# Kernel tuning notes

Hardware: AMD Instinct MI355X
Metric: run time of the kernel (lower is better)

Reference implementation:

```python
import jax, jax.numpy as jnp
import numpy as np

N_TOKENS = 8192
D_MODEL = 1024
D_HIDDEN = 2 * D_MODEL
N_EXPERTS = 16
TOP_K = 2


def setup_inputs() -> dict:
    key = jax.random.key(0)
    ks = jax.random.split(key, 6)
    s_in = 1.0 / np.sqrt(D_MODEL)
    s_hid = 1.0 / np.sqrt(D_HIDDEN)
    return {
        "x": jax.random.normal(ks[0], (N_TOKENS, D_MODEL), dtype=jnp.float32),
        # gate: Linear(d_model, n_experts, bias=False); stored as [E, d] like torch weight
        "Wg": jax.random.uniform(ks[1], (N_EXPERTS, D_MODEL), jnp.float32, -s_in, s_in),
        # per-expert MLP params, stacked on leading expert axis; W laid out [in, out]
        "W1": jax.random.uniform(ks[2], (N_EXPERTS, D_MODEL, D_HIDDEN), jnp.float32, -s_in, s_in),
        "b1": jax.random.uniform(ks[3], (N_EXPERTS, D_HIDDEN), jnp.float32, -s_in, s_in),
        "W2": jax.random.uniform(ks[4], (N_EXPERTS, D_HIDDEN, D_MODEL), jnp.float32, -s_hid, s_hid),
        "b2": jax.random.uniform(ks[5], (N_EXPERTS, D_MODEL), jnp.float32, -s_hid, s_hid),
    }


def reference(x, Wg, W1, b1, W2, b2):
    # Router: top-k logits, softmax over the k selected logits (in fp32)
    logits = x @ Wg.T                                  # [N, E]
    topk_vals, topk_idx = jax.lax.top_k(logits, TOP_K)  # [N, K]
    rw = jax.nn.softmax(topk_vals.astype(jnp.float32), axis=-1).astype(x.dtype)
    # Combine top-k weights into per-(token, expert) weights [N, E]
    cw = (jax.nn.one_hot(topk_idx, N_EXPERTS, dtype=x.dtype) * rw[..., None]).sum(axis=1)
    # Dense per-expert MLP, weighted combine (equivalent to gather/scatter index_add_)
    out = jnp.zeros_like(x)
    for e in range(N_EXPERTS):
        h = jax.nn.relu(x @ W1[e] + b1[e])             # [N, D_HIDDEN]
        out = out + (h @ W2[e] + b2[e]) * cw[:, e:e + 1]
    return out
```

## Files before the change

### kernel.cpp

```cpp
#include <hip/hip_runtime.h>
#include <hip/hip_bf16.h>
#include <stdint.h>

#define NTOK 8192
#define DM   1024
#define DH   2048
#define NE   16

#define NWRK  768
#define QCAP1 2048
#define QCAP2 1024

typedef float  f32x4  __attribute__((ext_vector_type(4)));
typedef __bf16 bf16x8 __attribute__((ext_vector_type(8)));

__device__ __forceinline__ unsigned short f2bf(float f) {
  union { __bf16 b; unsigned short u; } c; c.b = (__bf16)f; return c.u;
}

__device__ __forceinline__ void glds16(const void* g, void* l) {
  __builtin_amdgcn_global_load_lds(
      (const __attribute__((address_space(1))) void*)g,
      (__attribute__((address_space(3))) void*)l, 16, 0, 0);
}

__global__ __launch_bounds__(256) void router_kernel(
    const float* __restrict__ x, const float* __restrict__ Wg,
    unsigned short* __restrict__ xb, int* __restrict__ eidx,
    float* __restrict__ ewt)
{
  const int lane = threadIdx.x & 63;
  const int wave = threadIdx.x >> 6;
  const int t = blockIdx.x * 4 + wave;
  const float* xr = x + (size_t)t * DM;

  float4 xv[4];
#pragma unroll
  for (int c = 0; c < 4; ++c)
    xv[c] = *(const float4*)(xr + c * 256 + lane * 4);

  unsigned short* xbr = xb + (size_t)t * DM;
#pragma unroll
  for (int c = 0; c < 4; ++c) {
    ushort4 u;
    u.x = f2bf(xv[c].x); u.y = f2bf(xv[c].y);
    u.z = f2bf(xv[c].z); u.w = f2bf(xv[c].w);
    *(ushort4*)(xbr + c * 256 + lane * 4) = u;
  }

  float acc[NE];
#pragma unroll
  for (int e = 0; e < NE; ++e) acc[e] = 0.f;
#pragma unroll
  for (int e = 0; e < NE; ++e) {
#pragma unroll
    for (int c = 0; c < 4; ++c) {
      float4 wv = *(const float4*)(Wg + e * DM + c * 256 + lane * 4);
      acc[e] += xv[c].x * wv.x + xv[c].y * wv.y + xv[c].z * wv.z + xv[c].w * wv.w;
    }
  }
#pragma unroll
  for (int e = 0; e < NE; ++e) {
    float v = acc[e];
    v += __shfl_xor(v, 1);  v += __shfl_xor(v, 2);  v += __shfl_xor(v, 4);
    v += __shfl_xor(v, 8);  v += __shfl_xor(v, 16); v += __shfl_xor(v, 32);
    acc[e] = v;
  }
  if (lane == 0) {
    float v0 = -1e30f; int i0 = 0;
#pragma unroll
    for (int e = 0; e < NE; ++e) if (acc[e] > v0) { v0 = acc[e]; i0 = e; }
    float v1 = -1e30f; int i1 = 0;
#pragma unroll
    for (int e = 0; e < NE; ++e) if (e != i0 && acc[e] > v1) { v1 = acc[e]; i1 = e; }
    float p = expf(v1 - v0);
    float s = 1.f / (1.f + p);
    eidx[2 * t] = i0; eidx[2 * t + 1] = i1;
    ewt[2 * t] = s;   ewt[2 * t + 1] = p * s;
  }
}

__global__ __launch_bounds__(1024) void plan_kernel(
    const int* __restrict__ eidx, const float* __restrict__ ewt,
    int* __restrict__ cnt, int* __restrict__ offv,
    int* __restrict__ tok, float* __restrict__ wtl,
    int* __restrict__ wl1, int* __restrict__ wl2,
    int* __restrict__ qn1, int* __restrict__ qn2,
    int* __restrict__ qc1, int* __restrict__ qc2)
{
  __shared__ int wcnt[16][NE];
  __shared__ int wbase[16][NE];
  __shared__ int offs[NE];
  __shared__ int s_nmt[NE];
  __shared__ int s_pnmt[NE + 1];

  const int tid  = threadIdx.x;
  const int wave = tid >> 6;
  const int lane = tid & 63;
  const unsigned long long below = (1ull << lane) - 1ull;

  int   pe[16];
  float pw[16];
  int   count[NE];
#pragma unroll
  for (int e = 0; e < NE; ++e) count[e] = 0;
#pragma unroll
  for (int r = 0; r < 16; ++r) {
    int p = wave * 1024 + r * 64 + lane;
    pe[r] = eidx[p];
    pw[r] = ewt[p];
#pragma unroll
    for (int e = 0; e < NE; ++e) {
      unsigned long long m = __ballot(pe[r] == e);
      count[e] += (int)__popcll(m);
    }
  }
  if (lane == 0) {
#pragma unroll
    for (int e = 0; e < NE; ++e) wcnt[wave][e] = count[e];
  }
  __syncthreads();

  if (tid == 0) {
    int s = 0;
    s_pnmt[0] = 0;
    for (int e = 0; e < NE; ++e) {
      offs[e] = s;
      int t = 0;
      for (int w = 0; w < 16; ++w) { wbase[w][e] = t; t += wcnt[w][e]; }
      cnt[e] = t; offv[e] = s; s += t;
      int nmt = (t + 127) >> 7;
      s_nmt[e] = nmt;
      s_pnmt[e + 1] = s_pnmt[e] + nmt;
    }
    offv[NE] = s;
  }
  __syncthreads();

  if (tid < 8) {
    qn1[tid] = (s_nmt[tid] + s_nmt[tid + 8]) * 16;
    qn2[tid] = (s_nmt[tid] + s_nmt[tid + 8]) * 8;
    qc1[tid] = 0;
    qc2[tid] = 0;
  }

  {
    const int totmt = s_pnmt[NE];
    const int T1 = totmt * 16;
    for (int i = tid; i < T1; i += 1024) {
      int gmt = i >> 4, p = i & 15;
      int e = 0;
      while (s_pnmt[e + 1] <= gmt) ++e;
      int mt  = gmt - s_pnmt[e];
      int nmt = s_nmt[e];
      int x    = e & 7;
      int base = (e < 8) ? 0 : s_nmt[e - 8] * 16;
      wl1[x * QCAP1 + base + p * nmt + mt] = (e << 16) | (mt << 8) | p;
    }
    const int T2 = totmt * 8;
    for (int i = tid; i < T2; i += 1024) {
      int gmt = i >> 3, p = i & 7;
      int e = 0;
      while (s_pnmt[e + 1] <= gmt) ++e;
      int mt  = gmt - s_pnmt[e];
      int nmt = s_nmt[e];
      int h0  = (nmt + 1) >> 1;
      int pos_e = (mt < h0) ? (p * h0 + mt)
                            : (h0 * 8 + p * (nmt - h0) + (mt - h0));
      int x    = e & 7;
      int base = (e < 8) ? 0 : s_nmt[e - 8] * 8;
      wl2[x * QCAP2 + base + pos_e] = (e << 16) | (mt << 8) | p;
    }
  }

  int run[NE];
#pragma unroll
  for (int e = 0; e < NE; ++e) run[e] = 0;
#pragma unroll
  for (int r = 0; r < 16; ++r) {
    int p = wave * 1024 + r * 64 + lane;
#pragma unroll
    for (int e = 0; e < NE; ++e) {
      unsigned long long m = __ballot(pe[r] == e);
      if (pe[r] == e) {
        int rank = (int)__popcll(m & below);
        int slot = offs[e] + wbase[wave][e] + run[e] + rank;
        tok[slot] = p >> 1;
        wtl[slot] = pw[r];
      }
      run[e] += (int)__popcll(m);
    }
  }
}

__global__ __launch_bounds__(256) void wprep_kernel(
    const float* __restrict__ W, unsigned short* __restrict__ WT,
    int K, int N)
{
  __shared__ float t[64][68];
  const int e = blockIdx.z;
  const int k0 = blockIdx.y * 64;
  const int n0 = blockIdx.x * 64;
  const int tid = threadIdx.x;
  const int tr = tid >> 2;
  const int tc = (tid & 3) * 16;
  const float* src = W + ((size_t)e * K + k0) * N + n0;
#pragma unroll
  for (int j = 0; j < 4; ++j) {
    float4 v = *(const float4*)(src + (size_t)tr * N + tc + j * 4);
    t[tc + j * 4 + 0][tr] = v.x;
    t[tc + j * 4 + 1][tr] = v.y;
    t[tc + j * 4 + 2][tr] = v.z;
    t[tc + j * 4 + 3][tr] = v.w;
  }
  __syncthreads();
  unsigned short* dst = WT + ((size_t)e * N + n0) * K + k0;
#pragma unroll
  for (int j = 0; j < 4; ++j) {
    float4 v = *(const float4*)(&t[tr][tc + j * 4]);
    ushort4 u;
    u.x = f2bf(v.x); u.y = f2bf(v.y); u.z = f2bf(v.z); u.w = f2bf(v.w);
    *(ushort4*)(dst + (size_t)tr * K + tc + j * 4) = u;
  }
}

template<int GATHER, int EPI, int KDIM, int NDIM, int QCAP>
__global__ __launch_bounds__(256, 3) void gemm_kernel(
    const unsigned short* __restrict__ Abase,
    const unsigned short* __restrict__ BT,
    const float* __restrict__ bias,
    const int* __restrict__ cnt, const int* __restrict__ offv,
    const int* __restrict__ tok, const float* __restrict__ wtl,
    const int* __restrict__ wl, const int* __restrict__ qn,
    int* __restrict__ qc, void* __restrict__ outp)
{
  __shared__ unsigned short Al[128 * 64];
  __shared__ unsigned short Bl[128 * 64];
  __shared__ int s_j;

  const int xcd = blockIdx.x & 7;
  const int* q_ = wl + xcd * QCAP;
  const int myqn = qn[xcd];

  const int tid  = threadIdx.x;
  const int lane = tid & 63;
  const int wave = tid >> 6;
  const int wr = wave >> 1;
  const int wc = wave & 1;

  const int lr = lane >> 3;
  const int lc = lane & 7;
  const int sc = (lc ^ lr) * 8;
  const int qq   = lane >> 4;
  const int ln15 = lane & 15;
  const int swz  = ln15 & 7;

  for (;;) {
    if (tid == 0) s_j = atomicAdd(&qc[xcd], 1);
    __syncthreads();
    const int j = s_j;
    if (j >= myqn) return;
    const int v = q_[j];

    const int e  = (v >> 16) & 0xff;
    const int m0 = ((v >> 8) & 0xff) * 128;
    const int n0 = (v & 0xff) * 128;
    const int count = cnt[e];
    const int o     = offv[e];

    const unsigned short* aptr[4];
    const unsigned short* bptr[4];
#pragma unroll
    for (int ii = 0; ii < 4; ++ii) {
      int i = wave * 4 + ii;
      int r = i * 8 + lr;
      int m = m0 + r; if (m > count - 1) m = count - 1;
      size_t arow = GATHER ? (size_t)tok[o + m] : (size_t)(o + m);
      aptr[ii] = Abase + arow * KDIM + sc;
      bptr[ii] = BT + ((size_t)e * NDIM + n0 + r) * KDIM + sc;
    }

    f32x4 acc[4][4];
#pragma unroll
    for (int a = 0; a < 4; ++a)
#pragma unroll
      for (int b = 0; b < 4; ++b) acc[a][b] = 0.f;

    for (int k0 = 0; k0 < KDIM; k0 += 64) {
#pragma unroll
      for (int ii = 0; ii < 4; ++ii) {
        int i = wave * 4 + ii;
        glds16(aptr[ii] + k0, &Al[i * 512]);
        glds16(bptr[ii] + k0, &Bl[i * 512]);
      }
      __syncthreads();
#pragma unroll
      for (int kk = 0; kk < 2; ++kk) {
        bf16x8 af[4], bg[4];
        const int ch = (kk * 4 + qq) ^ swz;
#pragma unroll
        for (int a = 0; a < 4; ++a) {
          int r = wr * 64 + a * 16 + ln15;
          af[a] = *(const bf16x8*)(&Al[r * 64 + ch * 8]);
        }
#pragma unroll
        for (int b = 0; b < 4; ++b) {
          int r = wc * 64 + b * 16 + ln15;
          bg[b] = *(const bf16x8*)(&Bl[r * 64 + ch * 8]);
        }
#pragma unroll
        for (int a = 0; a < 4; ++a)
#pragma unroll
          for (int b = 0; b < 4; ++b)
            acc[a][b] = __builtin_amdgcn_mfma_f32_16x16x32_bf16(af[a], bg[b], acc[a][b], 0, 0, 0);
      }
      __syncthreads();
    }

    float bn[4];
#pragma unroll
    for (int b = 0; b < 4; ++b)
      bn[b] = bias[(size_t)e * NDIM + n0 + wc * 64 + b * 16 + ln15];

    if (EPI == 0) {
      unsigned short* hout = (unsigned short*)outp;
#pragma unroll
      for (int a = 0; a < 4; ++a)
#pragma unroll
        for (int rg = 0; rg < 4; ++rg) {
          int r = wr * 64 + a * 16 + qq * 4 + rg;
          int m = m0 + r;
          if (m < count) {
            size_t slot = (size_t)(o + m);
#pragma unroll
            for (int b = 0; b < 4; ++b) {
              float v2 = acc[a][b][rg] + bn[b];
              v2 = v2 > 0.f ? v2 : 0.f;
              hout[slot * NDIM + n0 + wc * 64 + b * 16 + ln15] = f2bf(v2);
            }
          }
        }
    } else {
      float* obase = (float*)outp;
#pragma unroll
      for (int a = 0; a < 4; ++a)
#pragma unroll
        for (int rg = 0; rg < 4; ++rg) {
          int r = wr * 64 + a * 16 + qq * 4 + rg;
          int m = m0 + r;
          if (m < count) {
            int slot = o + m;
            int tk = tok[slot];
            float w = wtl[slot];
#pragma unroll
            for (int b = 0; b < 4; ++b) {
              float v2 = (acc[a][b][rg] + bn[b]) * w;
              atomicAdd(&obase[(size_t)tk * NDIM + n0 + wc * 64 + b * 16 + ln15], v2);
            }
          }
        }
    }
  }
}

extern "C" void kernel_launch(void* const* d_in, const int* in_sizes, int n_in,
                              void* d_out, int out_size, void* d_ws, size_t ws_size,
                              hipStream_t stream) {
  const float* x  = (const float*)d_in[0];
  const float* Wg = (const float*)d_in[1];
  const float* W1 = (const float*)d_in[2];
  const float* b1 = (const float*)d_in[3];
  const float* W2 = (const float*)d_in[4];
  const float* b2 = (const float*)d_in[5];

  constexpr size_t OFF_CNT  = 0;
  constexpr size_t OFF_OFF  = 256;
  constexpr size_t OFF_QN1  = 512;
  constexpr size_t OFF_QN2  = 544;
  constexpr size_t OFF_QC1  = 576;
  constexpr size_t OFF_QC2  = 608;
  constexpr size_t OFF_WL1  = 4096;
  constexpr size_t OFF_WL2  = OFF_WL1 + (size_t)8 * QCAP1 * 4;
  constexpr size_t OFF_EIDX = 131072;
  constexpr size_t OFF_EWT  = OFF_EIDX + (size_t)NTOK * 2 * 4;
  constexpr size_t OFF_TOK  = OFF_EWT  + (size_t)NTOK * 2 * 4;
  constexpr size_t OFF_WTL  = OFF_TOK  + (size_t)NTOK * 2 * 4;
  constexpr size_t OFF_XB   = (size_t)1 << 20;
  constexpr size_t OFF_W1T  = OFF_XB  + (size_t)NTOK * DM * 2;
  constexpr size_t OFF_W2T  = OFF_W1T + (size_t)NE * DM * DH * 2;
  constexpr size_t OFF_H    = OFF_W2T + (size_t)NE * DH * DM * 2;
  constexpr size_t REQ      = OFF_H   + (size_t)NTOK * 2 * DH * 2;

  if (ws_size < REQ) {
    hipMemsetAsync(d_out, 0, (size_t)out_size * 4, stream);
    return;
  }

  char* ws = (char*)d_ws;
  int*   cnt    = (int*)(ws + OFF_CNT);
  int*   offv   = (int*)(ws + OFF_OFF);
  int*   qn1    = (int*)(ws + OFF_QN1);
  int*   qn2    = (int*)(ws + OFF_QN2);
  int*   qc1    = (int*)(ws + OFF_QC1);
  int*   qc2    = (int*)(ws + OFF_QC2);
  int*   wl1    = (int*)(ws + OFF_WL1);
  int*   wl2    = (int*)(ws + OFF_WL2);
  int*   eidx   = (int*)(ws + OFF_EIDX);
  float* ewt    = (float*)(ws + OFF_EWT);
  int*   tok    = (int*)(ws + OFF_TOK);
  float* wtl    = (float*)(ws + OFF_WTL);
  unsigned short* xb   = (unsigned short*)(ws + OFF_XB);
  unsigned short* w1t  = (unsigned short*)(ws + OFF_W1T);
  unsigned short* w2t  = (unsigned short*)(ws + OFF_W2T);
  unsigned short* hbuf = (unsigned short*)(ws + OFF_H);

  hipMemsetAsync(d_out, 0, (size_t)out_size * 4, stream);

  router_kernel<<<NTOK / 4, 256, 0, stream>>>(x, Wg, xb, eidx, ewt);
  wprep_kernel<<<dim3(DH / 64, DM / 64, NE), 256, 0, stream>>>(W1, w1t, DM, DH);
  wprep_kernel<<<dim3(DM / 64, DH / 64, NE), 256, 0, stream>>>(W2, w2t, DH, DM);
  plan_kernel<<<1, 1024, 0, stream>>>(eidx, ewt, cnt, offv, tok, wtl,
                                      wl1, wl2, qn1, qn2, qc1, qc2);

  gemm_kernel<1, 0, DM, DH, QCAP1><<<NWRK, 256, 0, stream>>>(
      xb, w1t, b1, cnt, offv, tok, wtl, wl1, qn1, qc1, hbuf);
  gemm_kernel<0, 1, DH, DM, QCAP2><<<NWRK, 256, 0, stream>>>(
      hbuf, w2t, b2, cnt, offv, tok, wtl, wl2, qn2, qc2, (float*)d_out);
}
```

Before: 406.6 us.

## Use single-wave 64x64 GEMM tiles with register double-buffering, merge prep kernels

```diff
diff --git a/kernel.cpp b/kernel.cpp
--- a/kernel.cpp
+++ b/kernel.cpp
@@ -7,9 +7,9 @@
 #define DH   2048
 #define NE   16
 
-#define NWRK  768
-#define QCAP1 2048
-#define QCAP2 1024
+#define NWRK  3072
+#define QCAP1 8704
+#define QCAP2 4352
 
 typedef float  f32x4  __attribute__((ext_vector_type(4)));
 typedef __bf16 bf16x8 __attribute__((ext_vector_type(8)));
@@ -18,65 +18,101 @@
   union { __bf16 b; unsigned short u; } c; c.b = (__bf16)f; return c.u;
 }
 
-__device__ __forceinline__ void glds16(const void* g, void* l) {
-  __builtin_amdgcn_global_load_lds(
-      (const __attribute__((address_space(1))) void*)g,
-      (__attribute__((address_space(3))) void*)l, 16, 0, 0);
-}
-
-__global__ __launch_bounds__(256) void router_kernel(
+__global__ __launch_bounds__(256) void prep_kernel(
     const float* __restrict__ x, const float* __restrict__ Wg,
     unsigned short* __restrict__ xb, int* __restrict__ eidx,
-    float* __restrict__ ewt)
+    float* __restrict__ ewt,
+    const float* __restrict__ W1, unsigned short* __restrict__ w1t,
+    const float* __restrict__ W2, unsigned short* __restrict__ w2t)
 {
-  const int lane = threadIdx.x & 63;
-  const int wave = threadIdx.x >> 6;
-  const int t = blockIdx.x * 4 + wave;
-  const float* xr = x + (size_t)t * DM;
-
-  float4 xv[4];
-#pragma unroll
-  for (int c = 0; c < 4; ++c)
-    xv[c] = *(const float4*)(xr + c * 256 + lane * 4);
-
-  unsigned short* xbr = xb + (size_t)t * DM;
-#pragma unroll
-  for (int c = 0; c < 4; ++c) {
+  __shared__ float t[64][68];
+  const int bid = blockIdx.x;
+
+  if (bid < 2048) {
+    const int lane = threadIdx.x & 63;
+    const int wave = threadIdx.x >> 6;
+    const int tk = bid * 4 + wave;
+    const float* xr = x + (size_t)tk * DM;
+
+    float4 xv[4];
+#pragma unroll
+    for (int c = 0; c < 4; ++c)
+      xv[c] = *(const float4*)(xr + c * 256 + lane * 4);
+
+    unsigned short* xbr = xb + (size_t)tk * DM;
+#pragma unroll
+    for (int c = 0; c < 4; ++c) {
+      ushort4 u;
+      u.x = f2bf(xv[c].x); u.y = f2bf(xv[c].y);
+      u.z = f2bf(xv[c].z); u.w = f2bf(xv[c].w);
+      *(ushort4*)(xbr + c * 256 + lane * 4) = u;
+    }
+
+    float acc[NE];
+#pragma unroll
+    for (int e = 0; e < NE; ++e) acc[e] = 0.f;
+#pragma unroll
+    for (int e = 0; e < NE; ++e) {
+#pragma unroll
+      for (int c = 0; c < 4; ++c) {
+        float4 wv = *(const float4*)(Wg + e * DM + c * 256 + lane * 4);
+        acc[e] += xv[c].x * wv.x + xv[c].y * wv.y + xv[c].z * wv.z + xv[c].w * wv.w;
+      }
+    }
+#pragma unroll
+    for (int e = 0; e < NE; ++e) {
+      float v = acc[e];
+      v += __shfl_xor(v, 1);  v += __shfl_xor(v, 2);  v += __shfl_xor(v, 4);
+      v += __shfl_xor(v, 8);  v += __shfl_xor(v, 16); v += __shfl_xor(v, 32);
+      acc[e] = v;
+    }
+    if (lane == 0) {
+      float v0 = -1e30f; int i0 = 0;
+#pragma unroll
+      for (int e = 0; e < NE; ++e) if (acc[e] > v0) { v0 = acc[e]; i0 = e; }
+      float v1 = -1e30f; int i1 = 0;
+#pragma unroll
+      for (int e = 0; e < NE; ++e) if (e != i0 && acc[e] > v1) { v1 = acc[e]; i1 = e; }
+      float p = expf(v1 - v0);
+      float s = 1.f / (1.f + p);
+      eidx[2 * tk] = i0; eidx[2 * tk + 1] = i1;
+      ewt[2 * tk] = s;   ewt[2 * tk + 1] = p * s;
+    }
+    return;
+  }
+
+  const float* W; unsigned short* WT; int K, N, bx, by, bz;
+  if (bid < 2048 + 8192) {
+    int i = bid - 2048;
+    W = W1; WT = w1t; K = DM; N = DH;
+    bx = i & 31; by = (i >> 5) & 15; bz = i >> 9;
+  } else {
+    int i = bid - 10240;
+    W = W2; WT = w2t; K = DH; N = DM;
+    bx = i & 15; by = (i >> 4) & 31; bz = i >> 9;
+  }
+  const int k0 = by * 64;
+  const int n0 = bx * 64;
+  const int tid = threadIdx.x;
+  const int tr = tid >> 2;
+  const int tc = (tid & 3) * 16;
+  const float* src = W + ((size_t)bz * K + k0) * N + n0;
+#pragma unroll
+  for (int j = 0; j < 4; ++j) {
+    float4 v = *(const float4*)(src + (size_t)tr * N + tc + j * 4);
+    t[tc + j * 4 + 0][tr] = v.x;
+    t[tc + j * 4 + 1][tr] = v.y;
+    t[tc + j * 4 + 2][tr] = v.z;
+    t[tc + j * 4 + 3][tr] = v.w;
+  }
+  __syncthreads();
+  unsigned short* dst = WT + ((size_t)bz * N + n0) * K + k0;
+#pragma unroll
+  for (int j = 0; j < 4; ++j) {
+    float4 v = *(const float4*)(&t[tr][tc + j * 4]);
     ushort4 u;
-    u.x = f2bf(xv[c].x); u.y = f2bf(xv[c].y);
-    u.z = f2bf(xv[c].z); u.w = f2bf(xv[c].w);
-    *(ushort4*)(xbr + c * 256 + lane * 4) = u;
-  }
-
-  float acc[NE];
-#pragma unroll
-  for (int e = 0; e < NE; ++e) acc[e] = 0.f;
-#pragma unroll
-  for (int e = 0; e < NE; ++e) {
-#pragma unroll
-    for (int c = 0; c < 4; ++c) {
-      float4 wv = *(const float4*)(Wg + e * DM + c * 256 + lane * 4);
-      acc[e] += xv[c].x * wv.x + xv[c].y * wv.y + xv[c].z * wv.z + xv[c].w * wv.w;
-    }
-  }
-#pragma unroll
-  for (int e = 0; e < NE; ++e) {
-    float v = acc[e];
-    v += __shfl_xor(v, 1);  v += __shfl_xor(v, 2);  v += __shfl_xor(v, 4);
-    v += __shfl_xor(v, 8);  v += __shfl_xor(v, 16); v += __shfl_xor(v, 32);
-    acc[e] = v;
-  }
-  if (lane == 0) {
-    float v0 = -1e30f; int i0 = 0;
-#pragma unroll
-    for (int e = 0; e < NE; ++e) if (acc[e] > v0) { v0 = acc[e]; i0 = e; }
-    float v1 = -1e30f; int i1 = 0;
-#pragma unroll
-    for (int e = 0; e < NE; ++e) if (e != i0 && acc[e] > v1) { v1 = acc[e]; i1 = e; }
-    float p = expf(v1 - v0);
-    float s = 1.f / (1.f + p);
-    eidx[2 * t] = i0; eidx[2 * t + 1] = i1;
-    ewt[2 * t] = s;   ewt[2 * t + 1] = p * s;
+    u.x = f2bf(v.x); u.y = f2bf(v.y); u.z = f2bf(v.z); u.w = f2bf(v.w);
+    *(ushort4*)(dst + (size_t)tr * K + tc + j * 4) = u;
   }
 }
 
@@ -129,7 +165,7 @@
       int t = 0;
       for (int w = 0; w < 16; ++w) { wbase[w][e] = t; t += wcnt[w][e]; }
       cnt[e] = t; offv[e] = s; s += t;
-      int nmt = (t + 127) >> 7;
+      int nmt = (t + 63) >> 6;
       s_nmt[e] = nmt;
       s_pnmt[e + 1] = s_pnmt[e] + nmt;
     }
@@ -138,38 +174,38 @@
   __syncthreads();
 
   if (tid < 8) {
-    qn1[tid] = (s_nmt[tid] + s_nmt[tid + 8]) * 16;
-    qn2[tid] = (s_nmt[tid] + s_nmt[tid + 8]) * 8;
+    qn1[tid] = (s_nmt[tid] + s_nmt[tid + 8]) * 32;
+    qn2[tid] = (s_nmt[tid] + s_nmt[tid + 8]) * 16;
     qc1[tid] = 0;
     qc2[tid] = 0;
   }
 
   {
     const int totmt = s_pnmt[NE];
-    const int T1 = totmt * 16;
+    const int T1 = totmt * 32;
     for (int i = tid; i < T1; i += 1024) {
-      int gmt = i >> 4, p = i & 15;
+      int gmt = i >> 5, p = i & 31;
       int e = 0;
       while (s_pnmt[e + 1] <= gmt) ++e;
       int mt  = gmt - s_pnmt[e];
       int nmt = s_nmt[e];
-      int x    = e & 7;
-      int base = (e < 8) ? 0 : s_nmt[e - 8] * 16;
-      wl1[x * QCAP1 + base + p * nmt + mt] = (e << 16) | (mt << 8) | p;
-    }
-    const int T2 = totmt * 8;
+      int xx   = e & 7;
+      int base = (e < 8) ? 0 : s_nmt[e - 8] * 32;
+      wl1[xx * QCAP1 + base + p * nmt + mt] = (e << 24) | (mt << 12) | p;
+    }
+    const int T2 = totmt * 16;
     for (int i = tid; i < T2; i += 1024) {
-      int gmt = i >> 3, p = i & 7;
+      int gmt = i >> 4, p = i & 15;
       int e = 0;
       while (s_pnmt[e + 1] <= gmt) ++e;
       int mt  = gmt - s_pnmt[e];
       int nmt = s_nmt[e];
       int h0  = (nmt + 1) >> 1;
       int pos_e = (mt < h0) ? (p * h0 + mt)
-                            : (h0 * 8 + p * (nmt - h0) + (mt - h0));
-      int x    = e & 7;
-      int base = (e < 8) ? 0 : s_nmt[e - 8] * 8;
-      wl2[x * QCAP2 + base + pos_e] = (e << 16) | (mt << 8) | p;
+                            : (h0 * 16 + p * (nmt - h0) + (mt - h0));
+      int xx   = e & 7;
+      int base = (e < 8) ? 0 : s_nmt[e - 8] * 16;
+      wl2[xx * QCAP2 + base + pos_e] = (e << 24) | (mt << 12) | p;
     }
   }
 
@@ -193,39 +229,8 @@
   }
 }
 
-__global__ __launch_bounds__(256) void wprep_kernel(
-    const float* __restrict__ W, unsigned short* __restrict__ WT,
-    int K, int N)
-{
-  __shared__ float t[64][68];
-  const int e = blockIdx.z;
-  const int k0 = blockIdx.y * 64;
-  const int n0 = blockIdx.x * 64;
-  const int tid = threadIdx.x;
-  const int tr = tid >> 2;
-  const int tc = (tid & 3) * 16;
-  const float* src = W + ((size_t)e * K + k0) * N + n0;
-#pragma unroll
-  for (int j = 0; j < 4; ++j) {
-    float4 v = *(const float4*)(src + (size_t)tr * N + tc + j * 4);
-    t[tc + j * 4 + 0][tr] = v.x;
-    t[tc + j * 4 + 1][tr] = v.y;
-    t[tc + j * 4 + 2][tr] = v.z;
-    t[tc + j * 4 + 3][tr] = v.w;
-  }
-  __syncthreads();
-  unsigned short* dst = WT + ((size_t)e * N + n0) * K + k0;
-#pragma unroll
-  for (int j = 0; j < 4; ++j) {
-    float4 v = *(const float4*)(&t[tr][tc + j * 4]);
-    ushort4 u;
-    u.x = f2bf(v.x); u.y = f2bf(v.y); u.z = f2bf(v.z); u.w = f2bf(v.w);
-    *(ushort4*)(dst + (size_t)tr * K + tc + j * 4) = u;
-  }
-}
-
 template<int GATHER, int EPI, int KDIM, int NDIM, int QCAP>
-__global__ __launch_bounds__(256, 3) void gemm_kernel(
+__global__ __launch_bounds__(64, 3) void gemm_kernel(
     const unsigned short* __restrict__ Abase,
     const unsigned short* __restrict__ BT,
     const float* __restrict__ bias,
@@ -234,50 +239,35 @@
     const int* __restrict__ wl, const int* __restrict__ qn,
     int* __restrict__ qc, void* __restrict__ outp)
 {
-  __shared__ unsigned short Al[128 * 64];
-  __shared__ unsigned short Bl[128 * 64];
-  __shared__ int s_j;
-
-  const int xcd = blockIdx.x & 7;
-  const int* q_ = wl + xcd * QCAP;
+  const int xcd  = blockIdx.x & 7;
+  const int lane = threadIdx.x;
+  const int q    = lane >> 4;
+  const int ln15 = lane & 15;
   const int myqn = qn[xcd];
-
-  const int tid  = threadIdx.x;
-  const int lane = tid & 63;
-  const int wave = tid >> 6;
-  const int wr = wave >> 1;
-  const int wc = wave & 1;
-
-  const int lr = lane >> 3;
-  const int lc = lane & 7;
-  const int sc = (lc ^ lr) * 8;
-  const int qq   = lane >> 4;
-  const int ln15 = lane & 15;
-  const int swz  = ln15 & 7;
+  const int* q_  = wl + xcd * QCAP;
+  constexpr int KH = KDIM / 32;
 
   for (;;) {
-    if (tid == 0) s_j = atomicAdd(&qc[xcd], 1);
-    __syncthreads();
-    const int j = s_j;
+    int j = 0;
+    if (lane == 0) j = atomicAdd(&qc[xcd], 1);
+    j = __shfl(j, 0);
     if (j >= myqn) return;
     const int v = q_[j];
 
-    const int e  = (v >> 16) & 0xff;
-    const int m0 = ((v >> 8) & 0xff) * 128;
-    const int n0 = (v & 0xff) * 128;
+    const int e  = v >> 24;
+    const int m0 = ((v >> 12) & 0xfff) * 64;
+    const int n0 = (v & 0xfff) * 64;
     const int count = cnt[e];
     const int o     = offv[e];
 
-    const unsigned short* aptr[4];
-    const unsigned short* bptr[4];
-#pragma unroll
-    for (int ii = 0; ii < 4; ++ii) {
-      int i = wave * 4 + ii;
-      int r = i * 8 + lr;
-      int m = m0 + r; if (m > count - 1) m = count - 1;
+    const unsigned short* ap[4];
+    const unsigned short* bp[4];
+#pragma unroll
+    for (int a = 0; a < 4; ++a) {
+      int m = m0 + a * 16 + ln15; if (m > count - 1) m = count - 1;
       size_t arow = GATHER ? (size_t)tok[o + m] : (size_t)(o + m);
-      aptr[ii] = Abase + arow * KDIM + sc;
-      bptr[ii] = BT + ((size_t)e * NDIM + n0 + r) * KDIM + sc;
+      ap[a] = Abase + arow * KDIM + q * 8;
+      bp[a] = BT + ((size_t)e * NDIM + n0 + a * 16 + ln15) * KDIM + q * 8;
     }
 
     f32x4 acc[4][4];
@@ -286,41 +276,40 @@
 #pragma unroll
       for (int b = 0; b < 4; ++b) acc[a][b] = 0.f;
 
-    for (int k0 = 0; k0 < KDIM; k0 += 64) {
-#pragma unroll
-      for (int ii = 0; ii < 4; ++ii) {
-        int i = wave * 4 + ii;
-        glds16(aptr[ii] + k0, &Al[i * 512]);
-        glds16(bptr[ii] + k0, &Bl[i * 512]);
-      }
-      __syncthreads();
-#pragma unroll
-      for (int kk = 0; kk < 2; ++kk) {
-        bf16x8 af[4], bg[4];
-        const int ch = (kk * 4 + qq) ^ swz;
-#pragma unroll
-        for (int a = 0; a < 4; ++a) {
-          int r = wr * 64 + a * 16 + ln15;
-          af[a] = *(const bf16x8*)(&Al[r * 64 + ch * 8]);
-        }
-#pragma unroll
-        for (int b = 0; b < 4; ++b) {
-          int r = wc * 64 + b * 16 + ln15;
-          bg[b] = *(const bf16x8*)(&Bl[r * 64 + ch * 8]);
-        }
-#pragma unroll
-        for (int a = 0; a < 4; ++a)
-#pragma unroll
-          for (int b = 0; b < 4; ++b)
-            acc[a][b] = __builtin_amdgcn_mfma_f32_16x16x32_bf16(af[a], bg[b], acc[a][b], 0, 0, 0);
-      }
-      __syncthreads();
-    }
+    bf16x8 a0[4], b0[4], a1[4], b1[4];
+
+#define LOADH(A_, B_, H_) {                                               \
+    _Pragma("unroll")                                                     \
+    for (int a = 0; a < 4; ++a) {                                         \
+      A_[a] = *(const bf16x8*)(ap[a] + (H_) * 32);                        \
+      B_[a] = *(const bf16x8*)(bp[a] + (H_) * 32);                        \
+    } }
+#define MFMAH(A_, B_) {                                                   \
+    _Pragma("unroll")                                                     \
+    for (int a = 0; a < 4; ++a)                                           \
+      _Pragma("unroll")                                                   \
+      for (int b = 0; b < 4; ++b)                                         \
+        acc[a][b] = __builtin_amdgcn_mfma_f32_16x16x32_bf16(              \
+            A_[a], B_[b], acc[a][b], 0, 0, 0);                            \
+    }
+
+    LOADH(a0, b0, 0)
+    for (int kh = 0; kh < KH - 2; kh += 2) {
+      LOADH(a1, b1, kh + 1)
+      MFMAH(a0, b0)
+      LOADH(a0, b0, kh + 2)
+      MFMAH(a1, b1)
+    }
+    LOADH(a1, b1, KH - 1)
+    MFMAH(a0, b0)
+    MFMAH(a1, b1)
+#undef LOADH
+#undef MFMAH
 
     float bn[4];
 #pragma unroll
     for (int b = 0; b < 4; ++b)
-      bn[b] = bias[(size_t)e * NDIM + n0 + wc * 64 + b * 16 + ln15];
+      bn[b] = bias[(size_t)e * NDIM + n0 + b * 16 + ln15];
 
     if (EPI == 0) {
       unsigned short* hout = (unsigned short*)outp;
@@ -328,15 +317,14 @@
       for (int a = 0; a < 4; ++a)
 #pragma unroll
         for (int rg = 0; rg < 4; ++rg) {
-          int r = wr * 64 + a * 16 + qq * 4 + rg;
-          int m = m0 + r;
+          int m = m0 + a * 16 + q * 4 + rg;
           if (m < count) {
             size_t slot = (size_t)(o + m);
 #pragma unroll
             for (int b = 0; b < 4; ++b) {
               float v2 = acc[a][b][rg] + bn[b];
               v2 = v2 > 0.f ? v2 : 0.f;
-              hout[slot * NDIM + n0 + wc * 64 + b * 16 + ln15] = f2bf(v2);
+              hout[slot * NDIM + n0 + b * 16 + ln15] = f2bf(v2);
             }
           }
         }
@@ -346,8 +334,7 @@
       for (int a = 0; a < 4; ++a)
 #pragma unroll
         for (int rg = 0; rg < 4; ++rg) {
-          int r = wr * 64 + a * 16 + qq * 4 + rg;
-          int m = m0 + r;
+          int m = m0 + a * 16 + q * 4 + rg;
           if (m < count) {
             int slot = o + m;
             int tk = tok[slot];
@@ -355,7 +342,7 @@
 #pragma unroll
             for (int b = 0; b < 4; ++b) {
               float v2 = (acc[a][b][rg] + bn[b]) * w;
-              atomicAdd(&obase[(size_t)tk * NDIM + n0 + wc * 64 + b * 16 + ln15], v2);
+              atomicAdd(&obase[(size_t)tk * NDIM + n0 + b * 16 + ln15], v2);
             }
           }
         }
@@ -379,9 +366,9 @@
   constexpr size_t OFF_QN2  = 544;
   constexpr size_t OFF_QC1  = 576;
   constexpr size_t OFF_QC2  = 608;
-  constexpr size_t OFF_WL1  = 4096;
+  constexpr size_t OFF_WL1  = 8192;
   constexpr size_t OFF_WL2  = OFF_WL1 + (size_t)8 * QCAP1 * 4;
-  constexpr size_t OFF_EIDX = 131072;
+  constexpr size_t OFF_EIDX = OFF_WL2 + (size_t)8 * QCAP2 * 4;
   constexpr size_t OFF_EWT  = OFF_EIDX + (size_t)NTOK * 2 * 4;
   constexpr size_t OFF_TOK  = OFF_EWT  + (size_t)NTOK * 2 * 4;
   constexpr size_t OFF_WTL  = OFF_TOK  + (size_t)NTOK * 2 * 4;
@@ -390,6 +377,7 @@
   constexpr size_t OFF_W2T  = OFF_W1T + (size_t)NE * DM * DH * 2;
   constexpr size_t OFF_H    = OFF_W2T + (size_t)NE * DH * DM * 2;
   constexpr size_t REQ      = OFF_H   + (size_t)NTOK * 2 * DH * 2;
+  static_assert(OFF_WTL + (size_t)NTOK * 2 * 4 <= OFF_XB, "ws layout overlap");
 
   if (ws_size < REQ) {
     hipMemsetAsync(d_out, 0, (size_t)out_size * 4, stream);
@@ -416,14 +404,12 @@
 
   hipMemsetAsync(d_out, 0, (size_t)out_size * 4, stream);
 
-  router_kernel<<<NTOK / 4, 256, 0, stream>>>(x, Wg, xb, eidx, ewt);
-  wprep_kernel<<<dim3(DH / 64, DM / 64, NE), 256, 0, stream>>>(W1, w1t, DM, DH);
-  wprep_kernel<<<dim3(DM / 64, DH / 64, NE), 256, 0, stream>>>(W2, w2t, DH, DM);
+  prep_kernel<<<18432, 256, 0, stream>>>(x, Wg, xb, eidx, ewt, W1, w1t, W2, w2t);
   plan_kernel<<<1, 1024, 0, stream>>>(eidx, ewt, cnt, offv, tok, wtl,
                                       wl1, wl2, qn1, qn2, qc1, qc2);
 
-  gemm_kernel<1, 0, DM, DH, QCAP1><<<NWRK, 256, 0, stream>>>(
+  gemm_kernel<1, 0, DM, DH, QCAP1><<<NWRK, 64, 0, stream>>>(
       xb, w1t, b1, cnt, offv, tok, wtl, wl1, qn1, qc1, hbuf);
-  gemm_kernel<0, 1, DH, DM, QCAP2><<<NWRK, 256, 0, stream>>>(
+  gemm_kernel<0, 1, DH, DM, QCAP2><<<NWRK, 64, 0, stream>>>(
       hbuf, w2t, b2, cnt, offv, tok, wtl, wl2, qn2, qc2, (float*)d_out);
 }
```

Measured after the change: 853.4 us. 2.1x slower.

## Split-K second GEMM, fuse weight prep into plan kernel, add cross-XCD work stealing

Applied to the files above, without the earlier changes.

```diff
diff --git a/kernel.cpp b/kernel.cpp
--- a/kernel.cpp
+++ b/kernel.cpp
@@ -9,7 +9,7 @@
 
 #define NWRK  768
 #define QCAP1 2048
-#define QCAP2 1024
+#define QCAP2 2048
 
 typedef float  f32x4  __attribute__((ext_vector_type(4)));
 typedef __bf16 bf16x8 __attribute__((ext_vector_type(8)));
@@ -80,20 +80,62 @@
   }
 }
 
-__global__ __launch_bounds__(1024) void plan_kernel(
+__global__ __launch_bounds__(1024) void planprep_kernel(
     const int* __restrict__ eidx, const float* __restrict__ ewt,
     int* __restrict__ cnt, int* __restrict__ offv,
     int* __restrict__ tok, float* __restrict__ wtl,
     int* __restrict__ wl1, int* __restrict__ wl2,
     int* __restrict__ qn1, int* __restrict__ qn2,
-    int* __restrict__ qc1, int* __restrict__ qc2)
+    int* __restrict__ qc1, int* __restrict__ qc2,
+    const float* __restrict__ W1, unsigned short* __restrict__ w1t,
+    const float* __restrict__ W2, unsigned short* __restrict__ w2t)
 {
+  __shared__ float t[4][64][68];
   __shared__ int wcnt[16][NE];
   __shared__ int wbase[16][NE];
   __shared__ int offs[NE];
   __shared__ int s_nmt[NE];
   __shared__ int s_pnmt[NE + 1];
 
+  if (blockIdx.x != 0) {
+    const int idx = blockIdx.x - 1;
+    const int tg  = threadIdx.x >> 8;
+    const int t8  = threadIdx.x & 255;
+    const float* W; unsigned short* WT; int K, N, tt, bx, by;
+    if (idx < 2048) {
+      W = W1; WT = w1t; K = DM; N = DH;
+      tt = idx * 4 + tg;
+      int r = tt & 511; bx = r & 31; by = r >> 5;
+    } else {
+      W = W2; WT = w2t; K = DH; N = DM;
+      tt = (idx - 2048) * 4 + tg;
+      int r = tt & 511; bx = r & 15; by = r >> 4;
+    }
+    const int bz = tt >> 9;
+    const int k0 = by * 64, n0 = bx * 64;
+    const int tr = t8 >> 2;
+    const int tc = (t8 & 3) * 16;
+    const float* src = W + ((size_t)bz * K + k0) * N + n0;
+#pragma unroll
+    for (int j = 0; j < 4; ++j) {
+      float4 v = *(const float4*)(src + (size_t)tr * N + tc + j * 4);
+      t[tg][tc + j * 4 + 0][tr] = v.x;
+      t[tg][tc + j * 4 + 1][tr] = v.y;
+      t[tg][tc + j * 4 + 2][tr] = v.z;
+      t[tg][tc + j * 4 + 3][tr] = v.w;
+    }
+    __syncthreads();
+    unsigned short* dst = WT + ((size_t)bz * N + n0) * K + k0;
+#pragma unroll
+    for (int j = 0; j < 4; ++j) {
+      float4 v = *(const float4*)(&t[tg][tr][tc + j * 4]);
+      ushort4 u;
+      u.x = f2bf(v.x); u.y = f2bf(v.y); u.z = f2bf(v.z); u.w = f2bf(v.w);
+      *(ushort4*)(dst + (size_t)tr * K + tc + j * 4) = u;
+    }
+    return;
+  }
+
   const int tid  = threadIdx.x;
   const int wave = tid >> 6;
   const int lane = tid & 63;
@@ -126,10 +168,10 @@
     s_pnmt[0] = 0;
     for (int e = 0; e < NE; ++e) {
       offs[e] = s;
-      int t = 0;
-      for (int w = 0; w < 16; ++w) { wbase[w][e] = t; t += wcnt[w][e]; }
-      cnt[e] = t; offv[e] = s; s += t;
-      int nmt = (t + 127) >> 7;
+      int tcnt = 0;
+      for (int w = 0; w < 16; ++w) { wbase[w][e] = tcnt; tcnt += wcnt[w][e]; }
+      cnt[e] = tcnt; offv[e] = s; s += tcnt;
+      int nmt = (tcnt + 127) >> 7;
       s_nmt[e] = nmt;
       s_pnmt[e + 1] = s_pnmt[e] + nmt;
     }
@@ -139,7 +181,7 @@
 
   if (tid < 8) {
     qn1[tid] = (s_nmt[tid] + s_nmt[tid + 8]) * 16;
-    qn2[tid] = (s_nmt[tid] + s_nmt[tid + 8]) * 8;
+    qn2[tid] = (s_nmt[tid] + s_nmt[tid + 8]) * 16;
     qc1[tid] = 0;
     qc2[tid] = 0;
   }
@@ -153,23 +195,22 @@
       while (s_pnmt[e + 1] <= gmt) ++e;
       int mt  = gmt - s_pnmt[e];
       int nmt = s_nmt[e];
-      int x    = e & 7;
+      int xx   = e & 7;
       int base = (e < 8) ? 0 : s_nmt[e - 8] * 16;
-      wl1[x * QCAP1 + base + p * nmt + mt] = (e << 16) | (mt << 8) | p;
-    }
-    const int T2 = totmt * 8;
+      wl1[xx * QCAP1 + base + p * nmt + mt] = (e << 16) | (mt << 8) | p;
+    }
+    const int T2 = totmt * 16;
     for (int i = tid; i < T2; i += 1024) {
-      int gmt = i >> 3, p = i & 7;
+      int gmt = i >> 4, sub = i & 15;
       int e = 0;
       while (s_pnmt[e + 1] <= gmt) ++e;
       int mt  = gmt - s_pnmt[e];
       int nmt = s_nmt[e];
-      int h0  = (nmt + 1) >> 1;
-      int pos_e = (mt < h0) ? (p * h0 + mt)
-                            : (h0 * 8 + p * (nmt - h0) + (mt - h0));
-      int x    = e & 7;
-      int base = (e < 8) ? 0 : s_nmt[e - 8] * 8;
-      wl2[x * QCAP2 + base + pos_e] = (e << 16) | (mt << 8) | p;
+      int xx   = e & 7;
+      int base = (e < 8) ? 0 : s_nmt[e - 8] * 16;
+      int p = sub >> 1, kh = sub & 1;
+      wl2[xx * QCAP2 + base + sub * nmt + mt] =
+          (e << 16) | (mt << 8) | (kh << 4) | p;
     }
   }
 
@@ -193,38 +234,7 @@
   }
 }
 
-__global__ __launch_bounds__(256) void wprep_kernel(
-    const float* __restrict__ W, unsigned short* __restrict__ WT,
-    int K, int N)
-{
-  __shared__ float t[64][68];
-  const int e = blockIdx.z;
-  const int k0 = blockIdx.y * 64;
-  const int n0 = blockIdx.x * 64;
-  const int tid = threadIdx.x;
-  const int tr = tid >> 2;
-  const int tc = (tid & 3) * 16;
-  const float* src = W + ((size_t)e * K + k0) * N + n0;
-#pragma unroll
-  for (int j = 0; j < 4; ++j) {
-    float4 v = *(const float4*)(src + (size_t)tr * N + tc + j * 4);
-    t[tc + j * 4 + 0][tr] = v.x;
-    t[tc + j * 4 + 1][tr] = v.y;
-    t[tc + j * 4 + 2][tr] = v.z;
-    t[tc + j * 4 + 3][tr] = v.w;
-  }
-  __syncthreads();
-  unsigned short* dst = WT + ((size_t)e * N + n0) * K + k0;
-#pragma unroll
-  for (int j = 0; j < 4; ++j) {
-    float4 v = *(const float4*)(&t[tr][tc + j * 4]);
-    ushort4 u;
-    u.x = f2bf(v.x); u.y = f2bf(v.y); u.z = f2bf(v.z); u.w = f2bf(v.w);
-    *(ushort4*)(dst + (size_t)tr * K + tc + j * 4) = u;
-  }
-}
-
-template<int GATHER, int EPI, int KDIM, int NDIM, int QCAP>
+template<int GATHER, int EPI, int SPLITK, int KDIM, int NDIM, int QCAP>
 __global__ __launch_bounds__(256, 3) void gemm_kernel(
     const unsigned short* __restrict__ Abase,
     const unsigned short* __restrict__ BT,
@@ -236,11 +246,9 @@
 {
   __shared__ unsigned short Al[128 * 64];
   __shared__ unsigned short Bl[128 * 64];
-  __shared__ int s_j;
-
-  const int xcd = blockIdx.x & 7;
-  const int* q_ = wl + xcd * QCAP;
-  const int myqn = qn[xcd];
+  __shared__ int s_item;
+
+  const int xcd0 = blockIdx.x & 7;
 
   const int tid  = threadIdx.x;
   const int lane = tid & 63;
@@ -255,16 +263,28 @@
   const int ln15 = lane & 15;
   const int swz  = ln15 & 7;
 
+  int sx = 0;
   for (;;) {
-    if (tid == 0) s_j = atomicAdd(&qc[xcd], 1);
+    if (tid == 0) {
+      int it = -1;
+      while (sx < 8) {
+        int x = (xcd0 + sx) & 7;
+        int j = atomicAdd(&qc[x], 1);
+        if (j < qn[x]) { it = wl[x * QCAP + j]; break; }
+        ++sx;
+      }
+      s_item = it;
+    }
     __syncthreads();
-    const int j = s_j;
-    if (j >= myqn) return;
-    const int v = q_[j];
+    const int v = s_item;
+    if (v < 0) return;
 
     const int e  = (v >> 16) & 0xff;
     const int m0 = ((v >> 8) & 0xff) * 128;
-    const int n0 = (v & 0xff) * 128;
+    int n0, kbase;
+    if (SPLITK) { n0 = (v & 0xf) * 128; kbase = ((v >> 4) & 1) * (KDIM / 2); }
+    else        { n0 = (v & 0xff) * 128; kbase = 0; }
+    constexpr int KEFF = SPLITK ? KDIM / 2 : KDIM;
     const int count = cnt[e];
     const int o     = offv[e];
 
@@ -286,7 +306,7 @@
 #pragma unroll
       for (int b = 0; b < 4; ++b) acc[a][b] = 0.f;
 
-    for (int k0 = 0; k0 < KDIM; k0 += 64) {
+    for (int k0 = kbase; k0 < kbase + KEFF; k0 += 64) {
 #pragma unroll
       for (int ii = 0; ii < 4; ++ii) {
         int i = wave * 4 + ii;
@@ -321,6 +341,10 @@
 #pragma unroll
     for (int b = 0; b < 4; ++b)
       bn[b] = bias[(size_t)e * NDIM + n0 + wc * 64 + b * 16 + ln15];
+    if (SPLITK && kbase != 0) {
+#pragma unroll
+      for (int b = 0; b < 4; ++b) bn[b] = 0.f;
+    }
 
     if (EPI == 0) {
       unsigned short* hout = (unsigned short*)outp;
@@ -381,7 +405,7 @@
   constexpr size_t OFF_QC2  = 608;
   constexpr size_t OFF_WL1  = 4096;
   constexpr size_t OFF_WL2  = OFF_WL1 + (size_t)8 * QCAP1 * 4;
-  constexpr size_t OFF_EIDX = 131072;
+  constexpr size_t OFF_EIDX = OFF_WL2 + (size_t)8 * QCAP2 * 4;
   constexpr size_t OFF_EWT  = OFF_EIDX + (size_t)NTOK * 2 * 4;
   constexpr size_t OFF_TOK  = OFF_EWT  + (size_t)NTOK * 2 * 4;
   constexpr size_t OFF_WTL  = OFF_TOK  + (size_t)NTOK * 2 * 4;
@@ -390,6 +414,7 @@
   constexpr size_t OFF_W2T  = OFF_W1T + (size_t)NE * DM * DH * 2;
   constexpr size_t OFF_H    = OFF_W2T + (size_t)NE * DH * DM * 2;
   constexpr size_t REQ      = OFF_H   + (size_t)NTOK * 2 * DH * 2;
+  static_assert(OFF_WTL + (size_t)NTOK * 2 * 4 <= OFF_XB, "ws layout overlap");
 
   if (ws_size < REQ) {
     hipMemsetAsync(d_out, 0, (size_t)out_size * 4, stream);
@@ -417,13 +442,12 @@
   hipMemsetAsync(d_out, 0, (size_t)out_size * 4, stream);
 
   router_kernel<<<NTOK / 4, 256, 0, stream>>>(x, Wg, xb, eidx, ewt);
-  wprep_kernel<<<dim3(DH / 64, DM / 64, NE), 256, 0, stream>>>(W1, w1t, DM, DH);
-  wprep_kernel<<<dim3(DM / 64, DH / 64, NE), 256, 0, stream>>>(W2, w2t, DH, DM);
-  plan_kernel<<<1, 1024, 0, stream>>>(eidx, ewt, cnt, offv, tok, wtl,
-                                      wl1, wl2, qn1, qn2, qc1, qc2);
-
-  gemm_kernel<1, 0, DM, DH, QCAP1><<<NWRK, 256, 0, stream>>>(
+  planprep_kernel<<<4097, 1024, 0, stream>>>(
+      eidx, ewt, cnt, offv, tok, wtl, wl1, wl2, qn1, qn2, qc1, qc2,
+      W1, w1t, W2, w2t);
+
+  gemm_kernel<1, 0, 0, DM, DH, QCAP1><<<NWRK, 256, 0, stream>>>(
       xb, w1t, b1, cnt, offv, tok, wtl, wl1, qn1, qc1, hbuf);
-  gemm_kernel<0, 1, DH, DM, QCAP2><<<NWRK, 256, 0, stream>>>(
+  gemm_kernel<0, 1, 1, DH, DM, QCAP2><<<NWRK, 256, 0, stream>>>(
       hbuf, w2t, b2, cnt, offv, tok, wtl, wl2, qn2, qc2, (float*)d_out);
 }
```

New measurement: 1.158 ms. 2.85x slower.
